# Optimization experiments

Hardware: AMD Instinct MI355X
Metric: run time of the kernel (lower is better)

The kernel has to match this reference:

```python
import jax, jax.numpy as jnp
import numpy as np

EMBED_DIM = 1024
NUM_HEADS = 16
HEAD_DIM = EMBED_DIM // NUM_HEADS
B, T = 2, 2048


def setup_inputs() -> dict:
    key = jax.random.key(0)
    kx, kqkv, kout = jax.random.split(key, 3)
    x = jax.random.normal(kx, (B, T, EMBED_DIM), dtype=jnp.float32)
    # torch Linear(in, out, bias=False): y = x @ W.T, W ~ U(-1/sqrt(in), 1/sqrt(in)).
    # Store pre-transposed as (in, out) for direct matmul.
    bound = 1.0 / np.sqrt(EMBED_DIM)
    w_qkv = jax.random.uniform(kqkv, (EMBED_DIM, 3 * EMBED_DIM), dtype=jnp.float32, minval=-bound, maxval=bound)
    w_out = jax.random.uniform(kout, (EMBED_DIM, EMBED_DIM), dtype=jnp.float32, minval=-bound, maxval=bound)
    return {"x": x, "w_qkv": w_qkv, "w_out": w_out}


def reference(x, w_qkv, w_out):
    Bx, Tx, C = x.shape
    qkv = x @ w_qkv  # (B, T, 3C)
    q, k, v = jnp.split(qkv, 3, axis=-1)

    def split_heads(t):
        return t.reshape(Bx, Tx, NUM_HEADS, HEAD_DIM).transpose(0, 2, 1, 3)  # (B,H,T,hd)

    q, k, v = split_heads(q), split_heads(k), split_heads(v)
    scale = 1.0 / jnp.sqrt(jnp.float32(HEAD_DIM))
    scores = jnp.einsum("bhqd,bhkd->bhqk", q, k) * scale  # (B,H,T,T)
    causal = jnp.tril(jnp.ones((Tx, Tx), dtype=bool))  # True = keep
    scores = jnp.where(causal, scores, jnp.float32(-jnp.inf))
    weights = jax.nn.softmax(scores, axis=-1)
    out = jnp.einsum("bhqk,bhkd->bhqd", weights, v)  # (B,H,T,hd)
    out = out.transpose(0, 2, 1, 3).reshape(Bx, Tx, C)
    return out @ w_out
```

## Files before the change

### kernel.cpp

```cpp
#include <hip/hip_runtime.h>
#include <hip/hip_bf16.h>
#include <stdint.h>
#include <math.h>

#define B_ 2
#define T_ 2048
#define C_ 1024
#define H_ 16
#define HD_ 64
#define BT_ (B_*T_)
#define N1_ (3*C_)

typedef unsigned short u16;
typedef uint32_t u32;
typedef __attribute__((ext_vector_type(8))) short bf16x8;
typedef __attribute__((ext_vector_type(4))) float f32x4;
typedef __attribute__((ext_vector_type(16))) float f32x16;
typedef __attribute__((ext_vector_type(4))) unsigned int u32x4;

__device__ __forceinline__ u16 f2bf(float f) {
  __hip_bfloat16 h = __float2bfloat16(f);
  return *reinterpret_cast<u16*>(&h);
}
__device__ __forceinline__ float bf2f(u16 u) {
  u32 w = ((u32)u) << 16;
  return *reinterpret_cast<float*>(&w);
}
__device__ __forceinline__ u32 cvtpk(float lo, float hi) {
  u32 r;
  asm("v_cvt_pk_bf16_f32 %0, %1, %2" : "=v"(r) : "v"(lo), "v"(hi));
  return r;
}
__device__ __forceinline__ float exp2v(float x) {
  float r;
  asm("v_exp_f32 %0, %1" : "=v"(r) : "v"(x));
  return r;
}

__device__ __forceinline__ void gload_lds16(const void* g, void* l) {
  __builtin_amdgcn_global_load_lds(
      (const __attribute__((address_space(1))) uint32_t*)g,
      (__attribute__((address_space(3))) uint32_t*)l, 16, 0, 0);
}

#define BARX() do { asm volatile("" ::: "memory"); __builtin_amdgcn_s_barrier(); \
                    asm volatile("" ::: "memory"); } while (0)
#define LGKM0() do { asm volatile("s_waitcnt lgkmcnt(0)" ::: "memory"); \
                     __builtin_amdgcn_sched_barrier(0); } while (0)

__global__ __launch_bounds__(256) void prep_k(const float* __restrict__ x,
                                              const float* __restrict__ w_qkv,
                                              const float* __restrict__ w_out,
                                              u16* __restrict__ xb,
                                              u16* __restrict__ wqkvT,
                                              u16* __restrict__ woutT) {
  __shared__ float tile[32][33];
  int bid = blockIdx.x;
  if (bid < 4096) {
    int idx = bid * 1024 + threadIdx.x * 4;
    float4 v = *reinterpret_cast<const float4*>(x + idx);
    u16 tmp[4] = {f2bf(v.x), f2bf(v.y), f2bf(v.z), f2bf(v.w)};
    *reinterpret_cast<uint2*>(xb + idx) = *reinterpret_cast<const uint2*>(tmp);
    return;
  }
  const float* w;
  u16* wt;
  int N, tb;
  if (bid < 7168) { tb = bid - 4096; w = w_qkv; wt = wqkvT; N = N1_; }
  else            { tb = bid - 7168; w = w_out; wt = woutT; N = C_;  }
  int nx = N >> 5;
  int n0 = (tb % nx) * 32, k0 = (tb / nx) * 32;
  int tx = threadIdx.x & 31, ty = threadIdx.x >> 5;
#pragma unroll
  for (int i = 0; i < 4; i++)
    tile[ty + i*8][tx] = w[(size_t)(k0 + ty + i*8) * N + n0 + tx];
  __syncthreads();
#pragma unroll
  for (int i = 0; i < 4; i++)
    wt[(size_t)(n0 + ty + i*8) * 1024 + k0 + tx] = f2bf(tile[tx][ty + i*8]);
}

__global__ __launch_bounds__(512, 2) void gemm256(const u16* __restrict__ A, const u16* __restrict__ Bt,
                                                  u16* __restrict__ Cc) {
  __shared__ u16 As[2][256*64];
  __shared__ u16 Bs[2][192*64];
  int tid = threadIdx.x, w = tid >> 6, lane = tid & 63;
  int m0 = blockIdx.y * 256, n0 = blockIdx.x * 192;
  int wm = (w >> 2) * 128, wn = (w & 3) * 48;
  f32x4 acc[8][3] = {};

  size_t aoff[4];
  size_t boff[3];
#pragma unroll
  for (int i = 0; i < 4; i++) {
    int c = i*512 + tid, row = c >> 3;
    aoff[i] = (size_t)(m0 + row) * 1024 + (size_t)((((c & 7) ^ (row & 7))) * 8);
  }
#pragma unroll
  for (int i = 0; i < 3; i++) {
    int c = i*512 + tid, row = c >> 3;
    boff[i] = (size_t)(n0 + row) * 1024 + (size_t)((((c & 7) ^ (row & 7))) * 8);
  }
  int dstc = w * 1024;

  int r15 = lane & 15, kq = lane >> 4;
  int slot0 = (kq ^ (r15 & 7)) * 8;
  int abase = (wm + r15) * 64;
  int bbase = (wn + r15) * 64;

#pragma unroll
  for (int i = 0; i < 4; i++)
    gload_lds16(A + aoff[i], (char*)&As[0][0] + i*8192 + dstc);
#pragma unroll
  for (int i = 0; i < 3; i++)
    gload_lds16(Bt + boff[i], (char*)&Bs[0][0] + i*8192 + dstc);

  for (int t = 0; t < 16; ++t) {
    int buf = t & 1;
    const u16* Ab = &As[buf][0];
    const u16* Bb = &Bs[buf][0];
    int slot1 = slot0 ^ 32;
    bf16x8 af[8], bfv[3];

    asm volatile("s_waitcnt vmcnt(0)" ::: "memory");
    BARX();

#pragma unroll
    for (int nf = 0; nf < 3; nf++) bfv[nf] = *reinterpret_cast<const bf16x8*>(&Bb[bbase + nf*1024 + slot0]);
#pragma unroll
    for (int mf = 0; mf < 8; mf++) af[mf] = *reinterpret_cast<const bf16x8*>(&Ab[abase + mf*1024 + slot0]);
    if (t < 15) {
      int ko = (t + 1) * 64;
#pragma unroll
      for (int i = 0; i < 4; i++)
        gload_lds16(A + aoff[i] + ko, (char*)&As[buf ^ 1][0] + i*8192 + dstc);
#pragma unroll
      for (int i = 0; i < 3; i++)
        gload_lds16(Bt + boff[i] + ko, (char*)&Bs[buf ^ 1][0] + i*8192 + dstc);
    }
    BARX();
    LGKM0();
    __builtin_amdgcn_s_setprio(1);
#pragma unroll
    for (int mf = 0; mf < 8; mf++)
#pragma unroll
      for (int nf = 0; nf < 3; nf++)
        acc[mf][nf] = __builtin_amdgcn_mfma_f32_16x16x32_bf16(af[mf], bfv[nf], acc[mf][nf], 0, 0, 0);
    __builtin_amdgcn_s_setprio(0);

#pragma unroll
    for (int nf = 0; nf < 3; nf++) bfv[nf] = *reinterpret_cast<const bf16x8*>(&Bb[bbase + nf*1024 + slot1]);
#pragma unroll
    for (int mf = 0; mf < 8; mf++) af[mf] = *reinterpret_cast<const bf16x8*>(&Ab[abase + mf*1024 + slot1]);
    BARX();
    LGKM0();
    __builtin_amdgcn_s_setprio(1);
#pragma unroll
    for (int mf = 0; mf < 8; mf++)
#pragma unroll
      for (int nf = 0; nf < 3; nf++)
        acc[mf][nf] = __builtin_amdgcn_mfma_f32_16x16x32_bf16(af[mf], bfv[nf], acc[mf][nf], 0, 0, 0);
    __builtin_amdgcn_s_setprio(0);
  }

  int rg = kq * 4;
#pragma unroll
  for (int mf = 0; mf < 8; mf++)
#pragma unroll
    for (int nf = 0; nf < 3; nf++) {
      size_t basei = (size_t)(m0 + wm + mf*16 + rg) * N1_ + (size_t)(n0 + wn + nf*16 + r15);
#pragma unroll
      for (int r = 0; r < 4; r++)
        Cc[basei + (size_t)r * N1_] = f2bf(acc[mf][nf][r]);
    }
}

template<int OUTF32>
__global__ __launch_bounds__(256) void gemm_bt(const u16* __restrict__ A, const u16* __restrict__ Bt,
                                               void* __restrict__ Cv, int M, int N, int K) {
  __shared__ u16 As[2][128*32];
  __shared__ u16 Bs[2][128*32];
  int tid = threadIdx.x, wave = tid >> 6, lane = tid & 63;
  int m0 = blockIdx.y * 128, n0 = blockIdx.x * 128;
  int wm = (wave >> 1) * 64, wn = (wave & 1) * 64;
  f32x4 acc[4][4] = {};
  int srow = lane >> 2, scol = (lane & 3) * 8;
  int fro  = (lane & 15) * 32 + (lane >> 4) * 8;

  auto stage = [&](int k0, int buf) {
#pragma unroll
    for (int i = 0; i < 2; i++) {
      gload_lds16(A  + (size_t)(m0 + i*64 + wave*16 + srow) * K + k0 + scol, &As[buf][(i*64 + wave*16) * 32]);
      gload_lds16(Bt + (size_t)(n0 + i*64 + wave*16 + srow) * K + k0 + scol, &Bs[buf][(i*64 + wave*16) * 32]);
    }
  };

  stage(0, 0);
  int nk = K >> 5;
  for (int it = 0; it < nk; ++it) {
    int cur = it & 1;
    asm volatile("s_waitcnt vmcnt(0)" ::: "memory");
    BARX();
    bf16x8 af[4], bfr[4];
#pragma unroll
    for (int i = 0; i < 4; i++) af[i]  = *reinterpret_cast<const bf16x8*>(&As[cur][(wm + i*16)*32 + fro]);
#pragma unroll
    for (int j2 = 0; j2 < 4; j2++) bfr[j2] = *reinterpret_cast<const bf16x8*>(&Bs[cur][(wn + j2*16)*32 + fro]);
    if (it + 1 < nk) stage((it + 1) << 5, cur ^ 1);
    BARX();
    LGKM0();
    __builtin_amdgcn_s_setprio(1);
#pragma unroll
    for (int i = 0; i < 4; i++)
#pragma unroll
      for (int j2 = 0; j2 < 4; j2++)
        acc[i][j2] = __builtin_amdgcn_mfma_f32_16x16x32_bf16(af[i], bfr[j2], acc[i][j2], 0, 0, 0);
    __builtin_amdgcn_s_setprio(0);
  }
  int rg = (lane >> 4) * 4, cq = lane & 15;
#pragma unroll
  for (int i = 0; i < 4; i++)
#pragma unroll
    for (int j2 = 0; j2 < 4; j2++) {
      size_t basei = (size_t)(m0 + wm + i*16 + rg) * N + (size_t)(n0 + wn + j2*16 + cq);
#pragma unroll
      for (int r = 0; r < 4; r++) {
        if constexpr (OUTF32) ((float*)Cv)[basei + (size_t)r * N] = acc[i][j2][r];
        else                  ((u16*)Cv)[basei + (size_t)r * N]   = f2bf(acc[i][j2][r]);
      }
    }
}

__global__ __launch_bounds__(192, 2) void attn_kernel(const u16* __restrict__ qkv, u16* __restrict__ attnout) {
  __shared__ u16 Sm[3][4096];
  int tid = threadIdx.x;
  int w = tid >> 6, lane = tid & 63;
  int q31 = lane & 31, hi = lane >> 5;
  int lid = blockIdx.x;
  int xcd = lid & 7, j = lid >> 3;
  int bh = xcd * 4 + (j & 3);
  int p = j >> 2;
  int b = bh >> 4, h = bh & 15;
  const u16* base = qkv + (size_t)b * T_ * N1_;

  u16* Ks = Sm[w];
  u32* Vt32 = reinterpret_cast<u32*>(Sm[w] + 2048);

  const u16* ksrc = base + C_ + h*HD_ + (size_t)(lane >> 3) * N1_
                    + (size_t)(((lane & 7) ^ ((lane >> 3) & 7)) * 8);
  int kp2 = lane & 15, dc = (lane >> 4) * 16;
  int vcs = kp2 >> 2, vkl = kp2 & 3;
  int vflip = (lane >> 4) & 1;
  const u16* vsrc = base + 2*C_ + h*HD_ + (size_t)(2*kp2) * N1_ + dc;
  const float QSC = 0.125f * 1.44269504088896f;
  int swr = (q31 >> 1) & 3;
  int q31f = q31 ^ ((q31 >> 4) & 1);

  int sA = 63 - p, sB = p;
  int qgA = sA * 32 + q31, qgB = sB * 32 + q31;
  int nktU = sA + 1;

  bf16x8 qfA[4], qfB[4];
  {
    const u16* qrowA = base + (size_t)qgA * N1_ + h * HD_;
    const u16* qrowB = base + (size_t)qgB * N1_ + h * HD_;
#pragma unroll
    for (int kk = 0; kk < 4; kk++) {
      bf16x8 ra = *reinterpret_cast<const bf16x8*>(qrowA + kk*16 + hi*8);
      bf16x8 rb = *reinterpret_cast<const bf16x8*>(qrowB + kk*16 + hi*8);
      const u16* pa = (const u16*)&ra;
      const u16* pb = (const u16*)&rb;
      u32x4 qa, qb;
#pragma unroll
      for (int jj = 0; jj < 4; jj++) {
        qa[jj] = cvtpk(bf2f(pa[2*jj]) * QSC, bf2f(pa[2*jj+1]) * QSC);
        qb[jj] = cvtpk(bf2f(pb[2*jj]) * QSC, bf2f(pb[2*jj+1]) * QSC);
      }
      qfA[kk] = __builtin_bit_cast(bf16x8, qa);
      qfB[kk] = __builtin_bit_cast(bf16x8, qb);
    }
  }

  f32x16 oaccA[2] = {}, oaccB[2] = {};
  float lA = 0.f, lB = 0.f;

  bf16x8 vA[2], vB[2];
  {
    size_t off0 = (size_t)(w * 32) * N1_;
#pragma unroll
    for (int r = 0; r < 4; r++)
      gload_lds16(ksrc + off0 + (size_t)(8*r) * N1_, (char*)Ks + r*1024);
#pragma unroll
    for (int r = 0; r < 2; r++) {
      vA[r] = *reinterpret_cast<const bf16x8*>(vsrc + off0 + r*8);
      vB[r] = *reinterpret_cast<const bf16x8*>(vsrc + off0 + r*8 + N1_);
    }
  }

  for (int kt = w; kt < nktU; kt += 3) {
    int kb = kt * 32;
    bool lastown = (kt + 3 >= nktU);
    bool actB = (kt <= sB);

    asm volatile("s_waitcnt vmcnt(0)" ::: "memory");

#pragma unroll
    for (int r2 = 0; r2 < 2; r2++) {
      const u16* au = (const u16*)&vA[r2];
      const u16* bu = (const u16*)&vB[r2];
#pragma unroll
      for (int i = 0; i < 8; i++) {
        int d = dc + r2*8 + i;
        Vt32[(d ^ vflip)*16 + ((vcs ^ ((d>>1)&3)) << 2) + vkl] = (u32)au[i] | ((u32)bu[i] << 16);
      }
    }

    f32x16 stA = {}, stB = {};
    if (actB) {
#pragma unroll
      for (int kk = 0; kk < 4; kk++) {
        bf16x8 kf = *reinterpret_cast<const bf16x8*>(
            &Ks[q31*64 + ((((kk<<1) | hi) ^ (q31 & 7)) << 3)]);
        stA = __builtin_amdgcn_mfma_f32_32x32x16_bf16(kf, qfA[kk], stA, 0, 0, 0);
        stB = __builtin_amdgcn_mfma_f32_32x32x16_bf16(kf, qfB[kk], stB, 0, 0, 0);
      }
    } else {
#pragma unroll
      for (int kk = 0; kk < 4; kk++) {
        bf16x8 kf = *reinterpret_cast<const bf16x8*>(
            &Ks[q31*64 + ((((kk<<1) | hi) ^ (q31 & 7)) << 3)]);
        stA = __builtin_amdgcn_mfma_f32_32x32x16_bf16(kf, qfA[kk], stA, 0, 0, 0);
      }
    }
    asm volatile("s_waitcnt lgkmcnt(0)" ::: "memory");
    __builtin_amdgcn_sched_barrier(0);

    if (!lastown) {
      size_t off = (size_t)(kb + 96) * N1_;
#pragma unroll
      for (int r = 0; r < 4; r++)
        gload_lds16(ksrc + off + (size_t)(8*r) * N1_, (char*)Ks + r*1024);
#pragma unroll
      for (int r = 0; r < 2; r++) {
        vA[r] = *reinterpret_cast<const bf16x8*>(vsrc + off + r*8);
        vB[r] = *reinterpret_cast<const bf16x8*>(vsrc + off + r*8 + N1_);
      }
    }

    if (kt == sA) {
#pragma unroll
      for (int r = 0; r < 16; r++) {
        int keyg = kb + (r&3) + 8*(r>>2) + 4*hi;
        if (keyg > qgA) stA[r] = -__builtin_inff();
      }
    }
    {
      float ts = 0.f;
#pragma unroll
      for (int r = 0; r < 16; r++) {
        float pp = exp2v(stA[r]);
        stA[r] = pp;
        ts += pp;
      }
      lA += ts;
    }
    bf16x8 pfA0, pfA1;
    {
      u32 pk[8];
#pragma unroll
      for (int m = 0; m < 8; m++) pk[m] = cvtpk(stA[2*m], stA[2*m+1]);
      asm volatile("v_permlane32_swap_b32 %0, %1" : "+v"(pk[0]), "+v"(pk[2]));
      asm volatile("v_permlane32_swap_b32 %0, %1" : "+v"(pk[1]), "+v"(pk[3]));
      asm volatile("v_permlane32_swap_b32 %0, %1" : "+v"(pk[4]), "+v"(pk[6]));
      asm volatile("v_permlane32_swap_b32 %0, %1" : "+v"(pk[5]), "+v"(pk[7]));
      u32x4 f0 = { pk[0], pk[1], pk[2], pk[3] };
      u32x4 f1 = { pk[4], pk[5], pk[6], pk[7] };
      pfA0 = __builtin_bit_cast(bf16x8, f0);
      pfA1 = __builtin_bit_cast(bf16x8, f1);
    }

    if (actB) {
      if (kt == sB) {
#pragma unroll
        for (int r = 0; r < 16; r++) {
          int keyg = kb + (r&3) + 8*(r>>2) + 4*hi;
          if (keyg > qgB) stB[r] = -__builtin_inff();
        }
      }
      {
        float ts = 0.f;
#pragma unroll
        for (int r = 0; r < 16; r++) {
          float pp = exp2v(stB[r]);
          stB[r] = pp;
          ts += pp;
        }
        lB += ts;
      }
      bf16x8 pfB0, pfB1;
      {
        u32 pk[8];
#pragma unroll
        for (int m = 0; m < 8; m++) pk[m] = cvtpk(stB[2*m], stB[2*m+1]);
        asm volatile("v_permlane32_swap_b32 %0, %1" : "+v"(pk[0]), "+v"(pk[2]));
        asm volatile("v_permlane32_swap_b32 %0, %1" : "+v"(pk[1]), "+v"(pk[3]));
        asm volatile("v_permlane32_swap_b32 %0, %1" : "+v"(pk[4]), "+v"(pk[6]));
        asm volatile("v_permlane32_swap_b32 %0, %1" : "+v"(pk[5]), "+v"(pk[7]));
        u32x4 f0 = { pk[0], pk[1], pk[2], pk[3] };
        u32x4 f1 = { pk[4], pk[5], pk[6], pk[7] };
        pfB0 = __builtin_bit_cast(bf16x8, f0);
        pfB1 = __builtin_bit_cast(bf16x8, f1);
      }
#pragma unroll
      for (int dt = 0; dt < 2; dt++)
#pragma unroll
        for (int kc = 0; kc < 2; kc++) {
          int cs = (kc << 1) | hi;
          bf16x8 vf = *reinterpret_cast<const bf16x8*>(
              &Vt32[(32*dt + q31f)*16 + ((cs ^ swr) << 2)]);
          oaccA[dt] = __builtin_amdgcn_mfma_f32_32x32x16_bf16(vf, kc ? pfA1 : pfA0, oaccA[dt], 0, 0, 0);
          oaccB[dt] = __builtin_amdgcn_mfma_f32_32x32x16_bf16(vf, kc ? pfB1 : pfB0, oaccB[dt], 0, 0, 0);
        }
    } else {
#pragma unroll
      for (int dt = 0; dt < 2; dt++)
#pragma unroll
        for (int kc = 0; kc < 2; kc++) {
          int cs = (kc << 1) | hi;
          bf16x8 vf = *reinterpret_cast<const bf16x8*>(
              &Vt32[(32*dt + q31f)*16 + ((cs ^ swr) << 2)]);
          oaccA[dt] = __builtin_amdgcn_mfma_f32_32x32x16_bf16(vf, kc ? pfA1 : pfA0, oaccA[dt], 0, 0, 0);
        }
    }
  }
  lA += __shfl_xor(lA, 32);
  lB += __shfl_xor(lB, 32);

  __syncthreads();
  if (w) {
    float* park = (float*)Sm[w];
#pragma unroll
    for (int dt = 0; dt < 2; dt++)
#pragma unroll
      for (int r = 0; r < 16; r++) park[(dt*16 + r)*64 + lane] = oaccA[dt][r];
    float* ml = (float*)Sm[0];
    ml[(w-1)*64 + lane] = lA;
  }
  __syncthreads();
  if (w == 0) {
    const float* ml = (const float*)Sm[0];
    float linv = 1.f / (lA + ml[lane] + ml[64 + lane]);
    const float* p1 = (const float*)Sm[1];
    const float* p2 = (const float*)Sm[2];
    u16* orow = attnout + (size_t)(b*T_ + qgA) * C_ + h*HD_;
#pragma unroll
    for (int dt = 0; dt < 2; dt++)
#pragma unroll
      for (int m = 0; m < 8; m++) {
        int e0 = (dt*16 + 2*m)*64 + lane, e1 = e0 + 64;
        float v0 = (oaccA[dt][2*m]   + p1[e0] + p2[e0]) * linv;
        float v1 = (oaccA[dt][2*m+1] + p1[e1] + p2[e1]) * linv;
        int d = 32*dt + 2*(m&1) + 8*(m>>1) + 4*hi;
        *reinterpret_cast<u32*>(orow + d) = cvtpk(v0, v1);
      }
  }
  __syncthreads();
  if (w) {
    float* park = (float*)Sm[w];
#pragma unroll
    for (int dt = 0; dt < 2; dt++)
#pragma unroll
      for (int r = 0; r < 16; r++) park[(dt*16 + r)*64 + lane] = oaccB[dt][r];
    float* ml = (float*)Sm[0];
    ml[(w-1)*64 + lane] = lB;
  }
  __syncthreads();
  if (w == 0) {
    const float* ml = (const float*)Sm[0];
    float linv = 1.f / (lB + ml[lane] + ml[64 + lane]);
    const float* p1 = (const float*)Sm[1];
    const float* p2 = (const float*)Sm[2];
    u16* orow = attnout + (size_t)(b*T_ + qgB) * C_ + h*HD_;
#pragma unroll
    for (int dt = 0; dt < 2; dt++)
#pragma unroll
      for (int m = 0; m < 8; m++) {
        int e0 = (dt*16 + 2*m)*64 + lane, e1 = e0 + 64;
        float v0 = (oaccB[dt][2*m]   + p1[e0] + p2[e0]) * linv;
        float v1 = (oaccB[dt][2*m+1] + p1[e1] + p2[e1]) * linv;
        int d = 32*dt + 2*(m&1) + 8*(m>>1) + 4*hi;
        *reinterpret_cast<u32*>(orow + d) = cvtpk(v0, v1);
      }
  }
}

extern "C" void kernel_launch(void* const* d_in, const int* in_sizes, int n_in,
                              void* d_out, int out_size, void* d_ws, size_t ws_size,
                              hipStream_t stream) {
  const float* x     = (const float*)d_in[0];
  const float* w_qkv = (const float*)d_in[1];
  const float* w_out = (const float*)d_in[2];
  float* out = (float*)d_out;
  char* ws = (char*)d_ws;
  u16* xb    = (u16*)(ws);
  u16* wqkvT = (u16*)(ws + ((size_t)8  << 20));
  u16* woutT = (u16*)(ws + ((size_t)14 << 20));
  u16* qkvb  = (u16*)(ws + ((size_t)16 << 20));
  u16* attnb = (u16*)(ws + ((size_t)40 << 20));

  prep_k<<<8192, 256, 0, stream>>>(x, w_qkv, w_out, xb, wqkvT, woutT);
  gemm256<<<dim3(16, 16), 512, 0, stream>>>(xb, wqkvT, qkvb);
  attn_kernel<<<1024, 192, 0, stream>>>(qkvb, attnb);
  gemm_bt<1><<<dim3(C_/128, BT_/128), 256, 0, stream>>>(attnb, woutT, (void*)out, BT_, C_, C_);
}
```

Baseline: 102.9 us.

## Replace output-projection GEMM with 512-thread, K64-step, XOR-swizzled LDS kernel

Swaps the generic 256-thread output-projection GEMM for a specialized 512-thread kernel with 8 waves, each owning a 64x32 tile. It stages 64-wide K slices instead of 32, halving the number of barrier/load iterations, and XOR-swizzles the LDS layout to avoid bank conflicts on fragment reads. The shapes are hardcoded to 1024. Doubling the LDS footprint and using launch_bounds(512,1) may lower occupancy, and each wave now has fewer MFMAs per LDS read.

```diff
diff --git a/kernel.cpp b/kernel.cpp
--- a/kernel.cpp
+++ b/kernel.cpp
@@ -175,59 +175,91 @@
     }
 }
 
-template<int OUTF32>
-__global__ __launch_bounds__(256) void gemm_bt(const u16* __restrict__ A, const u16* __restrict__ Bt,
-                                               void* __restrict__ Cv, int M, int N, int K) {
-  __shared__ u16 As[2][128*32];
-  __shared__ u16 Bs[2][128*32];
-  int tid = threadIdx.x, wave = tid >> 6, lane = tid & 63;
+__global__ __launch_bounds__(512, 1) void gemm128(const u16* __restrict__ A, const u16* __restrict__ Bt,
+                                                  float* __restrict__ Co) {
+  __shared__ u16 As[2][128*64];
+  __shared__ u16 Bs[2][128*64];
+  int tid = threadIdx.x, w = tid >> 6, lane = tid & 63;
   int m0 = blockIdx.y * 128, n0 = blockIdx.x * 128;
-  int wm = (wave >> 1) * 64, wn = (wave & 1) * 64;
-  f32x4 acc[4][4] = {};
-  int srow = lane >> 2, scol = (lane & 3) * 8;
-  int fro  = (lane & 15) * 32 + (lane >> 4) * 8;
-
-  auto stage = [&](int k0, int buf) {
-#pragma unroll
-    for (int i = 0; i < 2; i++) {
-      gload_lds16(A  + (size_t)(m0 + i*64 + wave*16 + srow) * K + k0 + scol, &As[buf][(i*64 + wave*16) * 32]);
-      gload_lds16(Bt + (size_t)(n0 + i*64 + wave*16 + srow) * K + k0 + scol, &Bs[buf][(i*64 + wave*16) * 32]);
-    }
-  };
-
-  stage(0, 0);
-  int nk = K >> 5;
-  for (int it = 0; it < nk; ++it) {
-    int cur = it & 1;
+  int wm = (w >> 2) * 64, wn = (w & 3) * 32;
+  f32x4 acc[4][2] = {};
+
+  size_t aoff[2], boff[2];
+#pragma unroll
+  for (int i = 0; i < 2; i++) {
+    int c = i*512 + tid, row = c >> 3;
+    aoff[i] = (size_t)(m0 + row) * 1024 + (size_t)((((c & 7) ^ (row & 7))) * 8);
+    boff[i] = (size_t)(n0 + row) * 1024 + (size_t)((((c & 7) ^ (row & 7))) * 8);
+  }
+  int dstc = w * 1024;
+
+  int r15 = lane & 15, kq = lane >> 4;
+  int slot0 = (kq ^ (r15 & 7)) * 8;
+  int abase = (wm + r15) * 64;
+  int bbase = (wn + r15) * 64;
+
+#pragma unroll
+  for (int i = 0; i < 2; i++) {
+    gload_lds16(A  + aoff[i], (char*)&As[0][0] + i*8192 + dstc);
+    gload_lds16(Bt + boff[i], (char*)&Bs[0][0] + i*8192 + dstc);
+  }
+
+  for (int t = 0; t < 16; ++t) {
+    int buf = t & 1;
+    const u16* Ab = &As[buf][0];
+    const u16* Bb = &Bs[buf][0];
+    int slot1 = slot0 ^ 32;
+    bf16x8 af[4], bfv[2];
+
     asm volatile("s_waitcnt vmcnt(0)" ::: "memory");
     BARX();
-    bf16x8 af[4], bfr[4];
-#pragma unroll
-    for (int i = 0; i < 4; i++) af[i]  = *reinterpret_cast<const bf16x8*>(&As[cur][(wm + i*16)*32 + fro]);
-#pragma unroll
-    for (int j2 = 0; j2 < 4; j2++) bfr[j2] = *reinterpret_cast<const bf16x8*>(&Bs[cur][(wn + j2*16)*32 + fro]);
-    if (it + 1 < nk) stage((it + 1) << 5, cur ^ 1);
+
+#pragma unroll
+    for (int nf = 0; nf < 2; nf++) bfv[nf] = *reinterpret_cast<const bf16x8*>(&Bb[bbase + nf*1024 + slot0]);
+#pragma unroll
+    for (int mf = 0; mf < 4; mf++) af[mf] = *reinterpret_cast<const bf16x8*>(&Ab[abase + mf*1024 + slot0]);
+    if (t < 15) {
+      int ko = (t + 1) * 64;
+#pragma unroll
+      for (int i = 0; i < 2; i++) {
+        gload_lds16(A  + aoff[i] + ko, (char*)&As[buf ^ 1][0] + i*8192 + dstc);
+        gload_lds16(Bt + boff[i] + ko, (char*)&Bs[buf ^ 1][0] + i*8192 + dstc);
+      }
+    }
     BARX();
     LGKM0();
     __builtin_amdgcn_s_setprio(1);
 #pragma unroll
-    for (int i = 0; i < 4; i++)
-#pragma unroll
-      for (int j2 = 0; j2 < 4; j2++)
-        acc[i][j2] = __builtin_amdgcn_mfma_f32_16x16x32_bf16(af[i], bfr[j2], acc[i][j2], 0, 0, 0);
+    for (int mf = 0; mf < 4; mf++)
+#pragma unroll
+      for (int nf = 0; nf < 2; nf++)
+        acc[mf][nf] = __builtin_amdgcn_mfma_f32_16x16x32_bf16(af[mf], bfv[nf], acc[mf][nf], 0, 0, 0);
     __builtin_amdgcn_s_setprio(0);
-  }
-  int rg = (lane >> 4) * 4, cq = lane & 15;
-#pragma unroll
-  for (int i = 0; i < 4; i++)
-#pragma unroll
-    for (int j2 = 0; j2 < 4; j2++) {
-      size_t basei = (size_t)(m0 + wm + i*16 + rg) * N + (size_t)(n0 + wn + j2*16 + cq);
-#pragma unroll
-      for (int r = 0; r < 4; r++) {
-        if constexpr (OUTF32) ((float*)Cv)[basei + (size_t)r * N] = acc[i][j2][r];
-        else                  ((u16*)Cv)[basei + (size_t)r * N]   = f2bf(acc[i][j2][r]);
-      }
+
+#pragma unroll
+    for (int nf = 0; nf < 2; nf++) bfv[nf] = *reinterpret_cast<const bf16x8*>(&Bb[bbase + nf*1024 + slot1]);
+#pragma unroll
+    for (int mf = 0; mf < 4; mf++) af[mf] = *reinterpret_cast<const bf16x8*>(&Ab[abase + mf*1024 + slot1]);
+    BARX();
+    LGKM0();
+    __builtin_amdgcn_s_setprio(1);
+#pragma unroll
+    for (int mf = 0; mf < 4; mf++)
+#pragma unroll
+      for (int nf = 0; nf < 2; nf++)
+        acc[mf][nf] = __builtin_amdgcn_mfma_f32_16x16x32_bf16(af[mf], bfv[nf], acc[mf][nf], 0, 0, 0);
+    __builtin_amdgcn_s_setprio(0);
+  }
+
+  int rg = kq * 4;
+#pragma unroll
+  for (int mf = 0; mf < 4; mf++)
+#pragma unroll
+    for (int nf = 0; nf < 2; nf++) {
+      size_t basei = (size_t)(m0 + wm + mf*16 + rg) * C_ + (size_t)(n0 + wn + nf*16 + r15);
+#pragma unroll
+      for (int r = 0; r < 4; r++)
+        Co[basei + (size_t)r * C_] = acc[mf][nf][r];
     }
 }
 
@@ -511,5 +543,5 @@
   prep_k<<<8192, 256, 0, stream>>>(x, w_qkv, w_out, xb, wqkvT, woutT);
   gemm256<<<dim3(16, 16), 512, 0, stream>>>(xb, wqkvT, qkvb);
   attn_kernel<<<1024, 192, 0, stream>>>(qkvb, attnb);
-  gemm_bt<1><<<dim3(C_/128, BT_/128), 256, 0, stream>>>(attnb, woutT, (void*)out, BT_, C_, C_);
-}
+  gemm128<<<dim3(8, 32), 512, 0, stream>>>(attnb, woutT, out);
+}
```

New measurement: 100.9 us. Within noise of the previous version (-1.9%).
